# Optimization experiments

Hardware: AMD Instinct MI355X
Metric: run time of the kernel (lower is better)

The kernel has to match this reference:

```python
import jax, jax.numpy as jnp
import numpy as np

B, C, R = 64, 4096, 16
CQ = C // R            # 256, must equal D*H*W
D, H, W = 4, 8, 8      # D*H*W == CQ (required by the original module's bmm/view math)


def setup_inputs() -> dict:
    key = jax.random.key(0)
    ks = jax.random.split(key, 7)
    s = 0.02
    x = jax.random.normal(ks[0], (B, C, D, H, W), dtype=jnp.float32)
    Wq = jax.random.normal(ks[1], (CQ, C), dtype=jnp.float32) * s
    bq = jnp.zeros((CQ,), dtype=jnp.float32)
    Wk = jax.random.normal(ks[2], (CQ, C), dtype=jnp.float32) * s
    bk = jnp.zeros((CQ,), dtype=jnp.float32)
    Wv = jax.random.normal(ks[3], (C, C), dtype=jnp.float32) * s
    bv = jnp.zeros((C,), dtype=jnp.float32)
    return {"x": x, "Wq": Wq, "bq": bq, "Wk": Wk, "bk": bk, "Wv": Wv, "bv": bv}


def reference(x, Wq, bq, Wk, bk, Wv, bv):
    b, c, d, h, w = x.shape
    n = d * h * w                       # == C//reduction
    xf = x.reshape(b, c, n)             # [B, C, N]
    # 1x1 Conv3d == per-position linear over channels
    q = jnp.einsum('oc,bcn->bon', Wq, xf) + bq[None, :, None]   # [B, Cq, N]
    k = jnp.einsum('oc,bcn->bon', Wk, xf) + bk[None, :, None]   # [B, Cq, N]
    v = jnp.einsum('oc,bcn->bon', Wv, xf) + bv[None, :, None]   # [B, C,  N]
    # energy[b,i,j] = sum_n q[b,i,n] * k[b,j,n]  (unscaled channel attention)
    energy = jnp.einsum('bin,bjn->bij', q, k)                   # [B, Cq, Cq]
    attn = jax.nn.softmax(energy, axis=-1)                      # [B, Cq, Cq]
    # out = V @ attn^T : out[b,c,i] = sum_n v[b,c,n] * attn[b,i,n]
    out = jnp.einsum('bcn,bin->bci', v, attn)                   # [B, C, N] (N==Cq)
    return out.reshape(x.shape)
```

## Files before the change

kernel.cpp:

```cpp
#include <hip/hip_runtime.h>
#include <hip/hip_bf16.h>
#include <stdint.h>

#define Bsz  64
#define Cch  4096
#define Npos 256
#define CQn  256

typedef __attribute__((ext_vector_type(8))) short bf16x8;
typedef __attribute__((ext_vector_type(4))) short s16x4;
typedef __attribute__((ext_vector_type(4))) float f32x4;

static __device__ __forceinline__ unsigned short f2bf(float f){
  union { float f; uint32_t u; } v; v.f = f;
  uint32_t u = v.u;
  u += 0x7FFFu + ((u >> 16) & 1u);
  return (unsigned short)(u >> 16);
}
static __device__ __forceinline__ float bf2f(unsigned short h){
  union { uint32_t u; float f; } v; v.u = ((uint32_t)h) << 16; return v.f;
}
static __device__ __forceinline__ void gload_lds16(const unsigned short* g, unsigned short* lds){
  __builtin_amdgcn_global_load_lds((const __attribute__((address_space(1))) void*)g,
                                   (__attribute__((address_space(3))) void*)lds, 16, 0, 0);
}

__global__ __launch_bounds__(256)
void split_x_kernel(const float* __restrict__ x, unsigned short* __restrict__ Xcat){
  __shared__ float tile[64][65];
  const int b = blockIdx.z, c0 = blockIdx.x * 64, n0 = blockIdx.y * 64;
  const float* xp = x + (size_t)b * Cch * Npos;
  const int t = threadIdx.x;
  #pragma unroll
  for (int p = 0; p < 16; ++p){
    int idx = p * 256 + t;
    int c = idx >> 6, n = idx & 63;
    tile[c][n] = xp[(size_t)(c0 + c) * Npos + n0 + n];
  }
  __syncthreads();
  #pragma unroll
  for (int p = 0; p < 16; ++p){
    int idx = p * 256 + t;
    int n = idx >> 6, c = idx & 63;
    float v = tile[c][n];
    unsigned short hi = f2bf(v);
    unsigned short lo = f2bf(v - bf2f(hi));
    size_t base = ((size_t)(b * 256 + n0 + n) << 13) + (size_t)(c0 + c);
    Xcat[base]        = hi;
    Xcat[base + 4096] = lo;
  }
}

__global__ __launch_bounds__(256)
void prep_acat_kernel(const float* __restrict__ Wq, const float* __restrict__ Wk,
                      unsigned short* __restrict__ Acat){
  size_t i = (size_t)blockIdx.x * 256 + threadIdx.x;
  int m = (int)(i >> 12), c = (int)(i & 4095);
  float wv = (m < 256) ? Wq[i] : Wk[i - 1048576];
  unsigned short hi = f2bf(wv);
  unsigned short lo = f2bf(wv - bf2f(hi));
  Acat[((size_t)m << 13) + c]        = hi;
  Acat[((size_t)m << 13) + 4096 + c] = lo;
}

__global__ __launch_bounds__(256)
void cast_wv_kernel(const float* __restrict__ Wv, unsigned short* __restrict__ Wvh){
  size_t i = ((size_t)blockIdx.x * 256 + threadIdx.x) * 4;
  f32x4 v = *(const f32x4*)(Wv + i);
  s16x4 h;
  h[0] = (short)f2bf(v[0]); h[1] = (short)f2bf(v[1]);
  h[2] = (short)f2bf(v[2]); h[3] = (short)f2bf(v[3]);
  *(s16x4*)(Wvh + i) = h;
}

template<int MODE>
__global__ __launch_bounds__(256)
void gemm128(const unsigned short* __restrict__ A, int ldA,
             const unsigned short* __restrict__ Bm, int ldB,
             const float* __restrict__ Bf32,
             const float* __restrict__ biasQ, const float* __restrict__ biasK,
             float* __restrict__ outQ, float* __restrict__ outK,
             unsigned short* __restrict__ outBF,
             float* __restrict__ outF, const float* __restrict__ biasV,
             int K)
{
  __shared__ __align__(16) unsigned short As[128 * 64];
  __shared__ __align__(16) unsigned short Bs[128 * 64];
  const int t = threadIdx.x;
  const int w = t >> 6, l = t & 63;
  const int wr = w >> 1, wc = w & 1;
  const int nt = blockIdx.x, mt = blockIdx.y, bz = blockIdx.z;
  const int row0 = mt * 128, col0 = nt * 128;

  const unsigned short* Ab = A;
  const float* xb = Bf32;
  if constexpr (MODE == 1) {
    Ab = A + (size_t)bz * (CQn * Npos);
    xb = Bf32 + (size_t)bz * ((size_t)Cch * Npos);
  }

  f32x4 acc[4][4];
  #pragma unroll
  for (int i = 0; i < 4; ++i)
    #pragma unroll
    for (int j = 0; j < 4; ++j) acc[i][j] = (f32x4){0.f, 0.f, 0.f, 0.f};

  const int lr8 = l >> 3;
  const int lk8 = (l & 7) * 8;
  const int fl  = l & 15;
  const int fk  = (l >> 4) * 8;

  const int nsteps = K >> 6;
  for (int kt = 0; kt < nsteps; ++kt){
    const int k0 = kt << 6;
    __syncthreads();
    {
      int ak = k0;
      if constexpr (MODE == 0) ak = (k0 < 4096) ? k0 : k0 - 4096;
      const unsigned short* Ab2 = Ab + (size_t)row0 * ldA + ak + lk8;
      #pragma unroll
      for (int r = 0; r < 4; ++r){
        int rr = r * 32 + w * 8 + lr8;
        gload_lds16(Ab2 + (size_t)rr * ldA, &As[(r * 32 + w * 8) * 64]);
      }
    }
    if constexpr (MODE == 1){
      #pragma unroll
      for (int p = 0; p < 8; ++p){
        int c = p * 16 + (t >> 4);
        int slot = t & 15;
        f32x4 v = *(const f32x4*)(xb + (size_t)(col0 + c) * Npos + k0 + slot * 4);
        s16x4 h;
        h[0] = (short)f2bf(v[0]); h[1] = (short)f2bf(v[1]);
        h[2] = (short)f2bf(v[2]); h[3] = (short)f2bf(v[3]);
        *(s16x4*)&Bs[c * 64 + slot * 4] = h;
      }
    } else {
      int bk = k0;
      if constexpr (MODE == 0) bk = (k0 < 8192) ? k0 : k0 - 8192;
      const unsigned short* Bb2 = Bm + (size_t)col0 * ldB + bk + lk8;
      #pragma unroll
      for (int r = 0; r < 4; ++r){
        int rr = r * 32 + w * 8 + lr8;
        gload_lds16(Bb2 + (size_t)rr * ldB, &Bs[(r * 32 + w * 8) * 64]);
      }
    }
    __syncthreads();
    #pragma unroll
    for (int kk = 0; kk < 2; ++kk){
      bf16x8 af[4], bfr[4];
      #pragma unroll
      for (int mi = 0; mi < 4; ++mi)
        af[mi] = *(const bf16x8*)&As[(wr * 64 + mi * 16 + fl) * 64 + kk * 32 + fk];
      #pragma unroll
      for (int nj = 0; nj < 4; ++nj)
        bfr[nj] = *(const bf16x8*)&Bs[(wc * 64 + nj * 16 + fl) * 64 + kk * 32 + fk];
      #pragma unroll
      for (int mi = 0; mi < 4; ++mi)
        #pragma unroll
        for (int nj = 0; nj < 4; ++nj)
          acc[mi][nj] = __builtin_amdgcn_mfma_f32_16x16x32_bf16(af[mi], bfr[nj], acc[mi][nj], 0, 0, 0);
    }
  }

  const int lrow = (l >> 4) * 4;
  #pragma unroll
  for (int mi = 0; mi < 4; ++mi){
    #pragma unroll
    for (int nj = 0; nj < 4; ++nj){
      int col = col0 + wc * 64 + nj * 16 + fl;
      f32x4 v = acc[mi][nj];
      #pragma unroll
      for (int r = 0; r < 4; ++r){
        int row = row0 + wr * 64 + mi * 16 + lrow + r;
        if constexpr (MODE == 0){
          int b = col >> 8, n = col & 255;
          float bia = (row < 256) ? biasQ[row] : biasK[row - 256];
          float* dst = (row < 256) ? outQ : outK;
          dst[((size_t)b << 16) + ((size_t)(row & 255) << 8) + n] = v[r] + bia;
        } else if constexpr (MODE == 1){
          outBF[(size_t)bz * ((size_t)CQn * Cch) + (size_t)row * Cch + col] = f2bf(v[r]);
        } else {
          int b = col >> 8, i2 = col & 255;
          outF[(size_t)b * ((size_t)Cch * Npos) + (size_t)row * Npos + i2] = v[r] + biasV[row];
        }
      }
    }
  }
}

__global__ __launch_bounds__(256)
void energy_kernel(const float* __restrict__ q, const float* __restrict__ k,
                   float* __restrict__ e){
  const int b = blockIdx.z;
  const int i0 = blockIdx.y * 64, j0 = blockIdx.x * 64;
  const float* qb = q + ((size_t)b << 16);
  const float* kb = k + ((size_t)b << 16);
  float* eb = e + ((size_t)b << 16);
  __shared__ float Qs[64][33];
  __shared__ float Ks[64][33];
  const int t = threadIdx.x;
  const int tx = t & 15, ty = t >> 4;
  float accv[4][4];
  #pragma unroll
  for (int ii = 0; ii < 4; ++ii)
    #pragma unroll
    for (int jj = 0; jj < 4; ++jj) accv[ii][jj] = 0.f;

  for (int n0 = 0; n0 < 256; n0 += 32){
    __syncthreads();
    #pragma unroll
    for (int p = 0; p < 8; ++p){
      int idx = p * 256 + t;
      int r = idx >> 5, n = idx & 31;
      Qs[r][n] = qb[(size_t)(i0 + r) * 256 + n0 + n];
      Ks[r][n] = kb[(size_t)(j0 + r) * 256 + n0 + n];
    }
    __syncthreads();
    #pragma unroll
    for (int n = 0; n < 32; ++n){
      float a4[4], b4[4];
      #pragma unroll
      for (int ii = 0; ii < 4; ++ii) a4[ii] = Qs[ty * 4 + ii][n];
      #pragma unroll
      for (int jj = 0; jj < 4; ++jj) b4[jj] = Ks[tx * 4 + jj][n];
      #pragma unroll
      for (int ii = 0; ii < 4; ++ii)
        #pragma unroll
        for (int jj = 0; jj < 4; ++jj) accv[ii][jj] = fmaf(a4[ii], b4[jj], accv[ii][jj]);
    }
  }
  #pragma unroll
  for (int ii = 0; ii < 4; ++ii){
    f32x4 o;
    #pragma unroll
    for (int jj = 0; jj < 4; ++jj) o[jj] = accv[ii][jj];
    *(f32x4*)&eb[(size_t)(i0 + ty * 4 + ii) * 256 + j0 + tx * 4] = o;
  }
}

__global__ __launch_bounds__(256)
void softmax_kernel(const float* __restrict__ e, unsigned short* __restrict__ attn){
  const size_t row = blockIdx.x;
  const int t = threadIdx.x;
  float v = e[(row << 8) + t];
  float m = v;
  #pragma unroll
  for (int off = 32; off >= 1; off >>= 1) m = fmaxf(m, __shfl_xor(m, off));
  __shared__ float red[8];
  if ((t & 63) == 0) red[t >> 6] = m;
  __syncthreads();
  m = fmaxf(fmaxf(red[0], red[1]), fmaxf(red[2], red[3]));
  float p = __expf(v - m);
  float s = p;
  #pragma unroll
  for (int off = 32; off >= 1; off >>= 1) s += __shfl_xor(s, off);
  if ((t & 63) == 0) red[4 + (t >> 6)] = s;
  __syncthreads();
  s = red[4] + red[5] + red[6] + red[7];
  attn[(row << 8) + t] = f2bf(p / s);
}

extern "C" void kernel_launch(void* const* d_in, const int* in_sizes, int n_in,
                              void* d_out, int out_size, void* d_ws, size_t ws_size,
                              hipStream_t stream){
  const float* x  = (const float*)d_in[0];
  const float* Wq = (const float*)d_in[1];
  const float* bq = (const float*)d_in[2];
  const float* Wk = (const float*)d_in[3];
  const float* bk = (const float*)d_in[4];
  const float* Wv = (const float*)d_in[5];
  const float* bv = (const float*)d_in[6];

  char* ws = (char*)d_ws;
  unsigned short* Xcat = (unsigned short*)ws;
  unsigned short* zT   = (unsigned short*)ws;
  unsigned short* Acat = (unsigned short*)(ws + 268435456u);
  unsigned short* Wvh  = (unsigned short*)(ws + 268435456u + 8388608u);

  char* ob = (char*)d_out;
  float* q            = (float*)ob;
  float* k            = (float*)(ob + 16777216u);
  float* en           = (float*)(ob + 33554432u);
  unsigned short* atb = (unsigned short*)(ob + 50331648u);
  float* outF         = (float*)d_out;

  split_x_kernel<<<dim3(64, 4, 64), 256, 0, stream>>>(x, Xcat);
  prep_acat_kernel<<<8192, 256, 0, stream>>>(Wq, Wk, Acat);
  cast_wv_kernel<<<16384, 256, 0, stream>>>(Wv, Wvh);

  gemm128<0><<<dim3(128, 4, 1), 256, 0, stream>>>(
      Acat, 8192, Xcat, 8192, nullptr, bq, bk, q, k, nullptr, nullptr, nullptr, 12288);

  energy_kernel<<<dim3(4, 4, 64), 256, 0, stream>>>(q, k, en);
  softmax_kernel<<<16384, 256, 0, stream>>>(en, atb);

  gemm128<1><<<dim3(32, 2, 64), 256, 0, stream>>>(
      atb, 256, nullptr, 0, x, nullptr, nullptr, nullptr, nullptr, zT, nullptr, nullptr, 256);

  gemm128<2><<<dim3(128, 32, 1), 256, 0, stream>>>(
      Wvh, 4096, zT, 4096, nullptr, nullptr, nullptr, nullptr, nullptr, nullptr, outF, bv, 4096);
}
```

Baseline: 1.808 ms.

## Replace final V-projection GEMM with 256x256-tile 4-stage pipelined MFMA kernel

The last GEMM (Wv times zT, 4096x16384x4096) moves from the 128x128 generic kernel to a dedicated 256x256-tile kernel with 512 threads. It uses a 4-slot LDS ring filled by direct global-to-LDS loads, interleaves prefetches between MFMA phases with barriers and setprio, swizzles LDS addressing, and remaps block IDs for L2 locality. The goal is higher MFMA utilization and less global traffic per flop on the dominant GEMM. The trade-off is heavy register and LDS use (128KB LDS) and hand-tuned waitcnt and barrier logic that could hurt occupancy or correctness.

```diff
diff --git a/kernel.cpp b/kernel.cpp
--- a/kernel.cpp
+++ b/kernel.cpp
@@ -71,6 +71,111 @@
   h[0] = (short)f2bf(v[0]); h[1] = (short)f2bf(v[1]);
   h[2] = (short)f2bf(v[2]); h[3] = (short)f2bf(v[3]);
   *(s16x4*)(Wvh + i) = h;
+}
+
+__global__ __launch_bounds__(512, 2)
+void gemm256_g3(const unsigned short* __restrict__ Ag,
+                const unsigned short* __restrict__ Bg,
+                const float* __restrict__ bias,
+                float* __restrict__ outF)
+{
+  __shared__ __align__(16) unsigned short ldsA[4][8192];
+  __shared__ __align__(16) unsigned short ldsB[4][8192];
+  const int t0 = threadIdx.x;
+  const int l = t0 & 63, w = t0 >> 6;
+  const int wr = w >> 2, wc = w & 3;
+  const int bid = blockIdx.x;
+  const int sb = (bid & 7) * 128 + (bid >> 3);
+  const int row0 = (sb >> 6) * 256;
+  const int col0 = (sb & 63) * 256;
+
+  const int sRow = l >> 2;
+  const int sK   = 8 * ((l & 3) ^ ((l >> 3) & 3));
+  const unsigned short* aSrc = Ag + (size_t)(row0 + w * 16 + sRow) * 4096 + sK;
+  const unsigned short* bSrc = Bg + (size_t)(col0 + w * 16 + sRow) * 4096 + sK;
+  const size_t halfStride = (size_t)128 * 4096;
+
+  const int fl  = l & 15, g = l >> 4;
+  const int swz = (l >> 1) & 3;
+  const int aOff = (wr * 128 + fl) * 32 + 8 * (g ^ swz);
+  const int bOff = (wc * 64  + fl) * 32 + 8 * (g ^ swz);
+
+  f32x4 acc[8][4];
+  #pragma unroll
+  for (int i = 0; i < 8; ++i)
+    #pragma unroll
+    for (int j = 0; j < 4; ++j) acc[i][j] = (f32x4){0.f, 0.f, 0.f, 0.f};
+
+  for (int ss = 0; ss < 3; ++ss){
+    const int k0 = ss * 32;
+    gload_lds16(aSrc + k0,              &ldsA[ss][(w * 16) * 32]);
+    gload_lds16(aSrc + halfStride + k0, &ldsA[ss][(128 + w * 16) * 32]);
+    gload_lds16(bSrc + k0,              &ldsB[ss][(w * 16) * 32]);
+    gload_lds16(bSrc + halfStride + k0, &ldsB[ss][(128 + w * 16) * 32]);
+  }
+
+  for (int t = 0; t < 128; ++t){
+    const int slot  = t & 3;
+    const int pslot = (t + 3) & 3;
+    const int pk0   = ((t + 3 < 128) ? (t + 3) : 127) * 32;
+    const unsigned short* As = ldsA[slot];
+    const unsigned short* Bs = ldsB[slot];
+
+    asm volatile("s_waitcnt vmcnt(8)" ::: "memory");
+    asm volatile("s_barrier" ::: "memory");
+
+    bf16x8 bfr[4];
+    #pragma unroll
+    for (int nj = 0; nj < 4; ++nj)
+      bfr[nj] = *(const bf16x8*)&Bs[bOff + nj * 512];
+    bf16x8 af[4];
+    #pragma unroll
+    for (int mi = 0; mi < 4; ++mi)
+      af[mi] = *(const bf16x8*)&As[aOff + mi * 512];
+    gload_lds16(aSrc + pk0,              &ldsA[pslot][(w * 16) * 32]);
+    gload_lds16(aSrc + halfStride + pk0, &ldsA[pslot][(128 + w * 16) * 32]);
+
+    asm volatile("s_barrier" ::: "memory");
+    __builtin_amdgcn_s_setprio(1);
+    #pragma unroll
+    for (int mi = 0; mi < 4; ++mi)
+      #pragma unroll
+      for (int nj = 0; nj < 4; ++nj)
+        acc[mi][nj] = __builtin_amdgcn_mfma_f32_16x16x32_bf16(af[mi], bfr[nj], acc[mi][nj], 0, 0, 0);
+    __builtin_amdgcn_s_setprio(0);
+
+    asm volatile("s_barrier" ::: "memory");
+    #pragma unroll
+    for (int mi = 0; mi < 4; ++mi)
+      af[mi] = *(const bf16x8*)&As[aOff + (4 + mi) * 512];
+    gload_lds16(bSrc + pk0,              &ldsB[pslot][(w * 16) * 32]);
+    gload_lds16(bSrc + halfStride + pk0, &ldsB[pslot][(128 + w * 16) * 32]);
+
+    asm volatile("s_barrier" ::: "memory");
+    __builtin_amdgcn_s_setprio(1);
+    #pragma unroll
+    for (int mi = 0; mi < 4; ++mi)
+      #pragma unroll
+      for (int nj = 0; nj < 4; ++nj)
+        acc[4 + mi][nj] = __builtin_amdgcn_mfma_f32_16x16x32_bf16(af[mi], bfr[nj], acc[4 + mi][nj], 0, 0, 0);
+    __builtin_amdgcn_s_setprio(0);
+  }
+  asm volatile("s_waitcnt vmcnt(0)" ::: "memory");
+
+  #pragma unroll
+  for (int mi = 0; mi < 8; ++mi){
+    #pragma unroll
+    for (int nj = 0; nj < 4; ++nj){
+      const int col = col0 + wc * 64 + nj * 16 + fl;
+      const int b = col >> 8, i2 = col & 255;
+      f32x4 v = acc[mi][nj];
+      #pragma unroll
+      for (int r = 0; r < 4; ++r){
+        const int row = row0 + wr * 128 + mi * 16 + g * 4 + r;
+        outF[(size_t)b * ((size_t)Cch * Npos) + (size_t)row * Npos + i2] = v[r] + bias[row];
+      }
+    }
+  }
 }
 
 template<int MODE>
@@ -298,6 +403,5 @@
   gemm128<1><<<dim3(32, 2, 64), 256, 0, stream>>>(
       atb, 256, nullptr, 0, x, nullptr, nullptr, nullptr, nullptr, zT, nullptr, nullptr, 256);
 
-  gemm128<2><<<dim3(128, 32, 1), 256, 0, stream>>>(
-      Wvh, 4096, zT, 4096, nullptr, nullptr, nullptr, nullptr, nullptr, nullptr, outF, bv, 4096);
-}
+  gemm256_g3<<<1024, 512, 0, stream>>>(Wvh, zT, bv, outF);
+}
```

Result: faster. 1.664 ms (-7.9%).
